# Kernel optimization log

Hardware: AMD Instinct MI355X
Metric: run time of the kernel (lower is better)

The kernel has to match this reference:

```python
import jax, jax.numpy as jnp
import numpy as np

B, M, EMBED, HEADS = 64, 1024, 1024, 8
HD = EMBED // HEADS  # 128
MID = 64             # att_mid_dim[1]
ALPHA = 1.3          # cfg.MODEL.BILINEAR.ELU_ALPHA (CELU)


def celu(x):
    return jax.nn.celu(x, alpha=ALPHA)


def group_norm(x, w, b, G=HEADS, eps=1e-5):
    # torch GroupNorm in source uses unbiased variance (ddof=1)
    N, C = x.shape
    xg = x.reshape(N, G, C // G)
    m = xg.mean(-1, keepdims=True)
    v = xg.var(-1, ddof=1, keepdims=True)
    xg = (xg - m) / jnp.sqrt(v + eps)
    return xg.reshape(N, C) * w + b


def setup_inputs() -> dict:
    key = jax.random.key(0)
    ks = jax.random.split(key, 16)
    s = 0.02
    return {
        "h_state": jax.random.normal(ks[0], (B, EMBED), jnp.float32),
        "att_feats": jax.random.normal(ks[1], (B, M, EMBED), jnp.float32),
        "att_mask": jnp.ones((B, M), jnp.float32),
        "p_att_feats": jax.random.normal(ks[2], (B, M, 2 * EMBED), jnp.float32),
        "Wq": jax.random.normal(ks[3], (EMBED, EMBED), jnp.float32) * s,
        "bq": jnp.zeros((EMBED,), jnp.float32),
        "gnw_q": jnp.ones((EMBED,), jnp.float32),
        "gnb_q": jnp.zeros((EMBED,), jnp.float32),
        "Wv1": jax.random.normal(ks[4], (EMBED, EMBED), jnp.float32) * s,
        "bv1": jnp.zeros((EMBED,), jnp.float32),
        "gnw_v1": jnp.ones((EMBED,), jnp.float32),
        "gnb_v1": jnp.zeros((EMBED,), jnp.float32),
        "Wb": jax.random.normal(ks[5], (HEADS, HD, MID), jnp.float32) * s,
        "bb": jax.random.normal(ks[6], (HEADS, MID), jnp.float32) * s,
        "Ws": jax.random.normal(ks[7], (HEADS, MID, 1), jnp.float32) * s,
        "bs": jax.random.normal(ks[8], (HEADS, 1), jnp.float32) * s,
        "Wc": jax.random.normal(ks[9], (HEADS, MID, HD), jnp.float32) * s,
        "bc": jax.random.normal(ks[10], (HEADS, HD), jnp.float32) * s,
        "Wt": jax.random.normal(ks[11], (2 * EMBED, EMBED), jnp.float32) * s,
        "bt": jnp.zeros((EMBED,), jnp.float32),
        "lnw": jnp.ones((EMBED,), jnp.float32),
        "lnb": jnp.zeros((EMBED,), jnp.float32),
    }


def reference(h_state, att_feats, att_mask, p_att_feats,
              Wq, bq, gnw_q, gnb_q, Wv1, bv1, gnw_v1, gnb_v1,
              Wb, bb, Ws, bs, Wc, bc, Wt, bt, lnw, lnb):
    b = h_state.shape[0]
    # precompute=True path: split p_att_feats into key / value2
    p_key = p_att_feats[..., :EMBED]
    p_value2 = p_att_feats[..., EMBED:]

    # q / v1 branches: Linear -> CELU -> GroupNorm
    q = group_norm(celu(h_state @ Wq + bq), gnw_q, gnb_q)    # [B, E]
    v1 = group_norm(celu(h_state @ Wv1 + bv1), gnw_v1, gnb_v1)

    p_query = q.reshape(b, HEADS, HD)[:, :, None, :]          # [B, H, 1, D]
    p_value1 = v1.reshape(b, HEADS, HD)[:, :, None, :]        # [B, H, 1, D]
    p_key = p_key.reshape(b, M, HEADS, HD).transpose(0, 2, 1, 3)     # [B, H, M, D]
    p_value2 = p_value2.reshape(b, M, HEADS, HD).transpose(0, 2, 1, 3)

    fusion = p_value2 * p_value1                              # [B, H, M, D]
    att_map = p_query * p_key                                 # [B, H, M, D]

    # attention_basic: MH_Linear + ReLU (dropout is identity at eval)
    am = jax.nn.relu(jnp.einsum('bhmi,hio->bhmo', att_map, Wb) + bb[None, :, None, :])  # [B,H,M,MID]

    mask = att_mask[:, None, :]                               # [B, 1, M]
    mext = mask[..., None]                                    # [B, 1, M, 1]
    att_map_pool = (am * mext).sum(-2) / mext.sum(-2)         # [B, H, MID]

    alpha_spatial = (jnp.einsum('bhmi,hio->bhmo', am, Ws) + bs[None, :, None, :])[..., 0]  # [B,H,M]
    alpha_spatial = jnp.where(mask == 0, -1e9, alpha_spatial)
    alpha_spatial = jax.nn.softmax(alpha_spatial, axis=-1)

    att = jnp.einsum('bhm,bhmd->bhd', alpha_spatial, fusion)  # [B, H, D]

    alpha_channel = jax.nn.sigmoid(jnp.einsum('bhi,hio->bho', att_map_pool, Wc) + bc[None])
    att = (att * alpha_channel).reshape(b, EMBED)

    out = jnp.concatenate([h_state, att], axis=-1) @ Wt + bt  # [B, E]
    mu = out.mean(-1, keepdims=True)
    var = out.var(-1, keepdims=True)
    out = (out - mu) / jnp.sqrt(var + 1e-5) * lnw + lnb
    return out
```

## Files before the change

kernel.cpp:

```cpp
#include <hip/hip_runtime.h>
#include <hip/hip_bf16.h>
#include <cmath>

#define NB 64
#define NM 1024
#define NE 1024
#define NH 8
#define NHD 128
#define NMID 64
#define CELU_ALPHA 1.3f

typedef __attribute__((ext_vector_type(8))) short bf16x8;
typedef __attribute__((ext_vector_type(4))) float f32x4;

__device__ __forceinline__ float celuf(float x) {
    return x > 0.f ? x : CELU_ALPHA * expm1f(x / CELU_ALPHA);
}

__device__ __forceinline__ short f2bf(float x) {
    __hip_bfloat16 b = __float2bfloat16(x);
    return *reinterpret_cast<short*>(&b);
}

__global__ __launch_bounds__(256) void a1_partial(
    const float* __restrict__ h, const float* __restrict__ Wq,
    const float* __restrict__ Wv1, float* __restrict__ partA)
{
    const int t = threadIdx.x;
    const int mat = blockIdx.x >> 8;
    const int kq = (blockIdx.x >> 5) & 7;
    const int cc = (blockIdx.x & 31) * 32;
    const int kbase = kq * 128;
    const float* __restrict__ W = mat ? Wv1 : Wq;

    __shared__ float hs[64][68];
    const int col = cc + (t & 31);
    const int rowg = t >> 5;

    float acc[8];
#pragma unroll
    for (int j = 0; j < 8; ++j) acc[j] = 0.f;

    for (int k0 = 0; k0 < 128; k0 += 64) {
        {
            const int r = t >> 2, b0 = (t & 3) * 16;
#pragma unroll
            for (int u = 0; u < 4; ++u) {
                float4 v = *(const float4*)&h[r * 1024 + kbase + k0 + b0 + 4 * u];
                *(float4*)&hs[r][b0 + 4 * u] = v;
            }
        }
        __syncthreads();
#pragma unroll 8
        for (int kl = 0; kl < 64; ++kl) {
            const float wv = W[(size_t)(kbase + k0 + kl) * 1024 + col];
#pragma unroll
            for (int j = 0; j < 8; ++j)
                acc[j] = fmaf(hs[rowg * 8 + j][kl], wv, acc[j]);
        }
        __syncthreads();
    }
    float* __restrict__ out = partA + (size_t)(mat * 8 + kq) * 65536;
#pragma unroll
    for (int j = 0; j < 8; ++j)
        out[(rowg * 8 + j) * 1024 + col] = acc[j];
}

__global__ __launch_bounds__(256) void a2_fused(
    const float* __restrict__ partA,
    const float* __restrict__ bq, const float* __restrict__ bv1,
    const float* __restrict__ gnw_q, const float* __restrict__ gnb_q,
    const float* __restrict__ gnw_v, const float* __restrict__ gnb_v,
    float* __restrict__ qbuf, float* __restrict__ v1buf)
{
    const int t = threadIdx.x;
    const int mat = blockIdx.x >> 6;
    const int row = blockIdx.x & 63;
    float* __restrict__ outb = mat ? v1buf : qbuf;
    const float* __restrict__ bias = mat ? bv1 : bq;
    const float* __restrict__ gw = mat ? gnw_v : gnw_q;
    const float* __restrict__ gb = mat ? gnb_v : gnb_q;

    float4 x = *(const float4*)&bias[t * 4];
#pragma unroll
    for (int kq = 0; kq < 8; ++kq) {
        const float4 p = *(const float4*)&partA[(size_t)(mat * 8 + kq) * 65536 + row * 1024 + t * 4];
        x.x += p.x; x.y += p.y; x.z += p.z; x.w += p.w;
    }
    x.x = celuf(x.x); x.y = celuf(x.y); x.z = celuf(x.z); x.w = celuf(x.w);

    float s = x.x + x.y + x.z + x.w;
#pragma unroll
    for (int m = 16; m >= 1; m >>= 1) s += __shfl_xor(s, m);
    const float mean = s * (1.f / 128.f);
    const float d0 = x.x - mean, d1 = x.y - mean, d2 = x.z - mean, d3 = x.w - mean;
    float ss = d0 * d0 + d1 * d1 + d2 * d2 + d3 * d3;
#pragma unroll
    for (int m = 16; m >= 1; m >>= 1) ss += __shfl_xor(ss, m);
    const float inv = rsqrtf(ss * (1.f / 127.f) + 1e-5f);
    const float4 w4 = *(const float4*)&gw[t * 4];
    const float4 b4 = *(const float4*)&gb[t * 4];
    float4 y;
    y.x = d0 * inv * w4.x + b4.x;
    y.y = d1 * inv * w4.y + b4.y;
    y.z = d2 * inv * w4.z + b4.z;
    y.w = d3 * inv * w4.w + b4.w;
    *(float4*)&outb[row * 1024 + t * 4] = y;
}

__global__ __launch_bounds__(256) void b0_wbq(
    const float* __restrict__ q, const float* __restrict__ Wb,
    short* __restrict__ wbq_g)
{
    const int bid = blockIdx.x;
    const int b = bid >> 3, h = bid & 7;
    const int t = threadIdx.x;
    __shared__ float q_lds[128];
    if (t < 128) q_lds[t] = q[b * 1024 + h * 128 + t];
    __syncthreads();

    const int o = t >> 2;
    const int i0 = (t & 3) * 32;
    union { short s[32]; uint4 q4[4]; } u;
#pragma unroll 8
    for (int v = 0; v < 32; ++v) {
        const int i = i0 + v;
        u.s[v] = f2bf(q_lds[i] * Wb[h * 8192 + i * 64 + o]);
    }
    uint4* dst = (uint4*)&wbq_g[(size_t)bid * 8192 + o * 128 + i0];
#pragma unroll
    for (int r = 0; r < 4; ++r) dst[r] = u.q4[r];
}

__global__ __launch_bounds__(256) void b_fused(
    const float* __restrict__ pat, const float* __restrict__ mask,
    const short* __restrict__ wbq_g,
    const float* __restrict__ bb, const float* __restrict__ Ws,
    const float* __restrict__ bs,
    float* __restrict__ pool_pt, float* __restrict__ esum_pt,
    float* __restrict__ av_pt)
{
    const int t = threadIdx.x;
    const int bid = blockIdx.x;
    const int b = bid >> 5;
    const int h = (bid >> 2) & 7;
    const int chunk = bid & 3;
    const int w = t >> 6;
    const int lane = t & 63;
    const int ln15 = lane & 15;
    const int lg = lane >> 4;
    const int dg = lane & 31;
    const int rwg = lane >> 5;

    __shared__ float mask_lds[256];
    __shared__ float e_lds[4][16];
    __shared__ float att_red[4][128];
    __shared__ float pool_red[4][64];
    __shared__ float esum_red[4];

    mask_lds[t] = mask[b * 1024 + chunk * 256 + t];

    const short* __restrict__ wb = wbq_g + (size_t)(bid >> 2) * 8192;
    bf16x8 bfr[4][4];
#pragma unroll
    for (int nt = 0; nt < 4; ++nt)
#pragma unroll
        for (int ks = 0; ks < 4; ++ks)
            bfr[nt][ks] = *(const bf16x8*)&wb[(nt * 16 + ln15) * 128 + ks * 32 + lg * 8];

    float wsr[4], bbr[4];
#pragma unroll
    for (int nt = 0; nt < 4; ++nt) {
        wsr[nt] = Ws[h * 64 + nt * 16 + ln15];
        bbr[nt] = bb[h * 64 + nt * 16 + ln15];
    }
    const float bsh = bs[h];
    float pool_part[4] = {0.f, 0.f, 0.f, 0.f};
    float esum_part = 0.f;
    float4 a4 = {0.f, 0.f, 0.f, 0.f};

    const float* __restrict__ patk = pat + (size_t)b * NM * 2048 + h * 128;
    const float* __restrict__ patv = patk + 1024;

    __syncthreads();

    for (int it = 0; it < 4; ++it) {
        const int ml0 = (w * 4 + it) * 16;
        const int m0 = chunk * 256 + ml0;

        const float* __restrict__ rowp = patk + (size_t)(m0 + ln15) * 2048 + lg * 8;
        bf16x8 af[4];
#pragma unroll
        for (int ks = 0; ks < 4; ++ks) {
            const float4 x = *(const float4*)(rowp + ks * 32);
            const float4 y = *(const float4*)(rowp + ks * 32 + 4);
            union { bf16x8 v; short s[8]; } u8;
            u8.s[0] = f2bf(x.x); u8.s[1] = f2bf(x.y);
            u8.s[2] = f2bf(x.z); u8.s[3] = f2bf(x.w);
            u8.s[4] = f2bf(y.x); u8.s[5] = f2bf(y.y);
            u8.s[6] = f2bf(y.z); u8.s[7] = f2bf(y.w);
            af[ks] = u8.v;
        }

        f32x4 acc[4];
#pragma unroll
        for (int nt = 0; nt < 4; ++nt) acc[nt] = (f32x4){0.f, 0.f, 0.f, 0.f};
#pragma unroll
        for (int ks = 0; ks < 4; ++ks)
#pragma unroll
            for (int nt = 0; nt < 4; ++nt)
                acc[nt] = __builtin_amdgcn_mfma_f32_16x16x32_bf16(af[ks], bfr[nt][ks], acc[nt], 0, 0, 0);

#pragma unroll
        for (int j = 0; j < 4; ++j) {
            const int ml = ml0 + lg * 4 + j;
            const float mk = mask_lds[ml];
            float sp = 0.f;
#pragma unroll
            for (int nt = 0; nt < 4; ++nt) {
                float a = acc[nt][j] + bbr[nt];
                a = fmaxf(a, 0.f);
                sp = fmaf(a, wsr[nt], sp);
                pool_part[nt] = fmaf(a, mk, pool_part[nt]);
            }
            sp += __shfl_xor(sp, 1);
            sp += __shfl_xor(sp, 2);
            sp += __shfl_xor(sp, 4);
            sp += __shfl_xor(sp, 8);
            if (ln15 == 0) {
                const float e = (mk == 0.f) ? 0.f : expf(sp + bsh);
                e_lds[w][lg * 4 + j] = e;
                esum_part += e;
            }
        }

        const float* __restrict__ vrow = patv + (size_t)(m0 + rwg) * 2048 + dg * 4;
#pragma unroll
        for (int r = 0; r < 8; ++r) {
            const float4 v = *(const float4*)(vrow + (size_t)(2 * r) * 2048);
            const float e = e_lds[w][rwg + 2 * r];
            a4.x = fmaf(e, v.x, a4.x);
            a4.y = fmaf(e, v.y, a4.y);
            a4.z = fmaf(e, v.z, a4.z);
            a4.w = fmaf(e, v.w, a4.w);
        }
    }

    a4.x += __shfl_xor(a4.x, 32);
    a4.y += __shfl_xor(a4.y, 32);
    a4.z += __shfl_xor(a4.z, 32);
    a4.w += __shfl_xor(a4.w, 32);
    if (lane < 32) *(float4*)&att_red[w][dg * 4] = a4;

#pragma unroll
    for (int nt = 0; nt < 4; ++nt) {
        float p = pool_part[nt];
        p += __shfl_xor(p, 16);
        p += __shfl_xor(p, 32);
        if (lane < 16) pool_red[w][nt * 16 + lane] = p;
    }

#pragma unroll
    for (int m = 32; m >= 1; m >>= 1) esum_part += __shfl_xor(esum_part, m);
    if (lane == 0) esum_red[w] = esum_part;
    __syncthreads();

    if (t < 128)
        av_pt[(size_t)bid * 128 + t] =
            att_red[0][t] + att_red[1][t] + att_red[2][t] + att_red[3][t];
    else if (t < 192)
        pool_pt[(size_t)bid * 64 + (t - 128)] =
            pool_red[0][t - 128] + pool_red[1][t - 128] + pool_red[2][t - 128] + pool_red[3][t - 128];
    else if (t == 192)
        esum_pt[bid] = esum_red[0] + esum_red[1] + esum_red[2] + esum_red[3];
}

__global__ __launch_bounds__(256) void b5_final(
    const float* __restrict__ pool_pt, const float* __restrict__ esum_pt,
    const float* __restrict__ av_pt, const float* __restrict__ mask,
    const float* __restrict__ Wc, const float* __restrict__ bc,
    const float* __restrict__ v1, float* __restrict__ att_out)
{
    const int t = threadIdx.x;
    const int bid = blockIdx.x;
    const int b = bid >> 3;
    const int h = bid & 7;
    const int w = t >> 6, lane = t & 63;

    __shared__ float red4[4];
    __shared__ float pool2[64];

    const float4 mk4 = *(const float4*)&mask[b * 1024 + t * 4];
    float msp = mk4.x + mk4.y + mk4.z + mk4.w;
#pragma unroll
    for (int m = 32; m >= 1; m >>= 1) msp += __shfl_xor(msp, m);
    if (lane == 0) red4[w] = msp;
    __syncthreads();
    const float msum = red4[0] + red4[1] + red4[2] + red4[3];

    if (t < 64) {
        const float pp = pool_pt[(size_t)(bid * 4) * 64 + t] + pool_pt[(size_t)(bid * 4 + 1) * 64 + t]
                       + pool_pt[(size_t)(bid * 4 + 2) * 64 + t] + pool_pt[(size_t)(bid * 4 + 3) * 64 + t];
        pool2[t] = pp / msum;
    }
    __syncthreads();

    if (t < 128) {
        const int d = t;
        const float av = av_pt[(size_t)(bid * 4) * 128 + d] + av_pt[(size_t)(bid * 4 + 1) * 128 + d]
                       + av_pt[(size_t)(bid * 4 + 2) * 128 + d] + av_pt[(size_t)(bid * 4 + 3) * 128 + d];
        const float esum = esum_pt[bid * 4] + esum_pt[bid * 4 + 1]
                         + esum_pt[bid * 4 + 2] + esum_pt[bid * 4 + 3];
        const float att = av / esum;
        float ac = bc[h * 128 + d];
#pragma unroll 8
        for (int o = 0; o < 64; ++o)
            ac = fmaf(pool2[o], Wc[h * 8192 + o * 128 + d], ac);
        const float sig = 1.f / (1.f + expf(-ac));
        att_out[b * 1024 + h * 128 + d] = att * sig * v1[b * 1024 + h * 128 + d];
    }
}

__global__ __launch_bounds__(256) void c1_partial(
    const float* __restrict__ h, const float* __restrict__ att,
    const float* __restrict__ Wt, float* __restrict__ part)
{
    const int t = threadIdx.x;
    const int kq = blockIdx.x >> 5;
    const int cc = (blockIdx.x & 31) * 32;
    const int col = cc + (t & 31);
    const int rowg = t >> 5;
    const float* __restrict__ x = (kq < 8) ? h : att;
    const int kbase = (kq & 7) * 128;

    __shared__ float xs[64][68];
    float acc[8];
#pragma unroll
    for (int j = 0; j < 8; ++j) acc[j] = 0.f;

    for (int k0 = 0; k0 < 128; k0 += 64) {
        {
            const int r = t >> 2, b0 = (t & 3) * 16;
#pragma unroll
            for (int u = 0; u < 4; ++u) {
                float4 v = *(const float4*)&x[r * 1024 + kbase + k0 + b0 + 4 * u];
                *(float4*)&xs[r][b0 + 4 * u] = v;
            }
        }
        __syncthreads();
#pragma unroll 8
        for (int kl = 0; kl < 64; ++kl) {
            const float wv = Wt[(size_t)(kq * 128 + k0 + kl) * 1024 + col];
#pragma unroll
            for (int j = 0; j < 8; ++j)
                acc[j] = fmaf(xs[rowg * 8 + j][kl], wv, acc[j]);
        }
        __syncthreads();
    }
#pragma unroll
    for (int j = 0; j < 8; ++j)
        part[(size_t)kq * 65536 + (rowg * 8 + j) * 1024 + col] = acc[j];
}

__global__ __launch_bounds__(256) void c2_ln(
    const float* __restrict__ part, const float* __restrict__ bt,
    const float* __restrict__ lnw, const float* __restrict__ lnb,
    float* __restrict__ out)
{
    const int t = threadIdx.x;
    const int row = blockIdx.x;
    const int w = t >> 6, lane = t & 63;
    __shared__ float red[4];

    float4 v = *(const float4*)&bt[t * 4];
#pragma unroll
    for (int qd = 0; qd < 16; ++qd) {
        const float4 p = *(const float4*)&part[(size_t)qd * 65536 + row * 1024 + t * 4];
        v.x += p.x; v.y += p.y; v.z += p.z; v.w += p.w;
    }
    float s = v.x + v.y + v.z + v.w;
#pragma unroll
    for (int m = 32; m >= 1; m >>= 1) s += __shfl_xor(s, m);
    if (lane == 0) red[w] = s;
    __syncthreads();
    const float mean = (red[0] + red[1] + red[2] + red[3]) * (1.f / 1024.f);
    __syncthreads();
    const float d0 = v.x - mean, d1 = v.y - mean, d2 = v.z - mean, d3 = v.w - mean;
    float ss = d0 * d0 + d1 * d1 + d2 * d2 + d3 * d3;
#pragma unroll
    for (int m = 32; m >= 1; m >>= 1) ss += __shfl_xor(ss, m);
    if (lane == 0) red[w] = ss;
    __syncthreads();
    const float var = (red[0] + red[1] + red[2] + red[3]) * (1.f / 1024.f);
    const float inv = rsqrtf(var + 1e-5f);
    const float4 w4 = *(const float4*)&lnw[t * 4];
    const float4 b4 = *(const float4*)&lnb[t * 4];
    float4 y;
    y.x = d0 * inv * w4.x + b4.x;
    y.y = d1 * inv * w4.y + b4.y;
    y.z = d2 * inv * w4.z + b4.z;
    y.w = d3 * inv * w4.w + b4.w;
    *(float4*)&out[row * 1024 + t * 4] = y;
}

extern "C" void kernel_launch(void* const* d_in, const int* in_sizes, int n_in,
                              void* d_out, int out_size, void* d_ws, size_t ws_size,
                              hipStream_t stream)
{
    const float* h_state  = (const float*)d_in[0];
    const float* att_mask = (const float*)d_in[2];
    const float* pat      = (const float*)d_in[3];
    const float* Wq       = (const float*)d_in[4];
    const float* bq       = (const float*)d_in[5];
    const float* gnw_q    = (const float*)d_in[6];
    const float* gnb_q    = (const float*)d_in[7];
    const float* Wv1      = (const float*)d_in[8];
    const float* bv1      = (const float*)d_in[9];
    const float* gnw_v1   = (const float*)d_in[10];
    const float* gnb_v1   = (const float*)d_in[11];
    const float* Wb       = (const float*)d_in[12];
    const float* bb       = (const float*)d_in[13];
    const float* Ws       = (const float*)d_in[14];
    const float* bs       = (const float*)d_in[15];
    const float* Wc       = (const float*)d_in[16];
    const float* bc       = (const float*)d_in[17];
    const float* Wt       = (const float*)d_in[18];
    const float* bt       = (const float*)d_in[19];
    const float* lnw      = (const float*)d_in[20];
    const float* lnb      = (const float*)d_in[21];
    float* out = (float*)d_out;

    float* ws      = (float*)d_ws;
    float* qbuf    = ws;
    float* v1buf   = ws + 65536;
    float* attb    = ws + 131072;
    float* parts   = ws + 196608;
    short* wbq_g   = (short*)(ws + 1245184);
    float* pool_pt = ws + 3342336;
    float* esum_pt = ws + 3473408;
    float* av_pt   = ws + 3475456;

    a1_partial<<<512, 256, 0, stream>>>(h_state, Wq, Wv1, parts);
    a2_fused<<<128, 256, 0, stream>>>(parts, bq, bv1, gnw_q, gnb_q, gnw_v1, gnb_v1,
                                      qbuf, v1buf);
    b0_wbq<<<512, 256, 0, stream>>>(qbuf, Wb, wbq_g);
    b_fused<<<2048, 256, 0, stream>>>(pat, att_mask, wbq_g, bb, Ws, bs,
                                      pool_pt, esum_pt, av_pt);
    b5_final<<<512, 256, 0, stream>>>(pool_pt, esum_pt, av_pt, att_mask,
                                      Wc, bc, v1buf, attb);
    c1_partial<<<512, 256, 0, stream>>>(h_state, attb, Wt, parts);
    c2_ln<<<64, 256, 0, stream>>>(parts, bt, lnw, lnb, out);
}
```

Baseline: 200.9 us.

## Retile small GEMMs, fuse group-norm into Wb prep, prefetch V rows

Result: faster. 160.8 us (-20.0%).

```diff
diff --git a/kernel.cpp b/kernel.cpp
--- a/kernel.cpp
+++ b/kernel.cpp
@@ -22,110 +22,118 @@
     return *reinterpret_cast<short*>(&b);
 }
 
-__global__ __launch_bounds__(256) void a1_partial(
+__global__ __launch_bounds__(256) void a1_tile(
     const float* __restrict__ h, const float* __restrict__ Wq,
     const float* __restrict__ Wv1, float* __restrict__ partA)
 {
     const int t = threadIdx.x;
-    const int mat = blockIdx.x >> 8;
-    const int kq = (blockIdx.x >> 5) & 7;
-    const int cc = (blockIdx.x & 31) * 32;
+    const int mat = blockIdx.x >> 7;
+    const int kq = (blockIdx.x >> 4) & 7;
+    const int cc = (blockIdx.x & 15) * 64;
     const int kbase = kq * 128;
     const float* __restrict__ W = mat ? Wv1 : Wq;
 
-    __shared__ float hs[64][68];
-    const int col = cc + (t & 31);
-    const int rowg = t >> 5;
-
-    float acc[8];
-#pragma unroll
-    for (int j = 0; j < 8; ++j) acc[j] = 0.f;
-
-    for (int k0 = 0; k0 < 128; k0 += 64) {
-        {
-            const int r = t >> 2, b0 = (t & 3) * 16;
-#pragma unroll
-            for (int u = 0; u < 4; ++u) {
-                float4 v = *(const float4*)&h[r * 1024 + kbase + k0 + b0 + 4 * u];
-                *(float4*)&hs[r][b0 + 4 * u] = v;
-            }
-        }
-        __syncthreads();
-#pragma unroll 8
-        for (int kl = 0; kl < 64; ++kl) {
-            const float wv = W[(size_t)(kbase + k0 + kl) * 1024 + col];
-#pragma unroll
-            for (int j = 0; j < 8; ++j)
-                acc[j] = fmaf(hs[rowg * 8 + j][kl], wv, acc[j]);
-        }
-        __syncthreads();
-    }
+    __shared__ float wl[128][64];
+    __shared__ float hl[64][132];
+
+#pragma unroll
+    for (int u = 0; u < 8; ++u) {
+        const int f = t + 256 * u;
+        const int row = f >> 4, c4 = f & 15;
+        *(float4*)&wl[row][c4 * 4] =
+            *(const float4*)&W[(size_t)(kbase + row) * 1024 + cc + c4 * 4];
+    }
+#pragma unroll
+    for (int u = 0; u < 8; ++u) {
+        const int f = t + 256 * u;
+        const int r = f >> 5, k4 = f & 31;
+        *(float4*)&hl[r][k4 * 4] = *(const float4*)&h[r * 1024 + kbase + k4 * 4];
+    }
+    __syncthreads();
+
+    const int r0 = (t >> 4) * 4;
+    const int c0 = (t & 15) * 4;
+    float acc[4][4];
+#pragma unroll
+    for (int i = 0; i < 4; ++i)
+#pragma unroll
+        for (int j = 0; j < 4; ++j) acc[i][j] = 0.f;
+
+#pragma unroll 4
+    for (int k = 0; k < 128; ++k) {
+        const float4 w4 = *(const float4*)&wl[k][c0];
+        const float h0 = hl[r0][k], h1 = hl[r0 + 1][k];
+        const float h2 = hl[r0 + 2][k], h3 = hl[r0 + 3][k];
+        acc[0][0] = fmaf(h0, w4.x, acc[0][0]); acc[0][1] = fmaf(h0, w4.y, acc[0][1]);
+        acc[0][2] = fmaf(h0, w4.z, acc[0][2]); acc[0][3] = fmaf(h0, w4.w, acc[0][3]);
+        acc[1][0] = fmaf(h1, w4.x, acc[1][0]); acc[1][1] = fmaf(h1, w4.y, acc[1][1]);
+        acc[1][2] = fmaf(h1, w4.z, acc[1][2]); acc[1][3] = fmaf(h1, w4.w, acc[1][3]);
+        acc[2][0] = fmaf(h2, w4.x, acc[2][0]); acc[2][1] = fmaf(h2, w4.y, acc[2][1]);
+        acc[2][2] = fmaf(h2, w4.z, acc[2][2]); acc[2][3] = fmaf(h2, w4.w, acc[2][3]);
+        acc[3][0] = fmaf(h3, w4.x, acc[3][0]); acc[3][1] = fmaf(h3, w4.y, acc[3][1]);
+        acc[3][2] = fmaf(h3, w4.z, acc[3][2]); acc[3][3] = fmaf(h3, w4.w, acc[3][3]);
+    }
+
     float* __restrict__ out = partA + (size_t)(mat * 8 + kq) * 65536;
 #pragma unroll
-    for (int j = 0; j < 8; ++j)
-        out[(rowg * 8 + j) * 1024 + col] = acc[j];
-}
-
-__global__ __launch_bounds__(256) void a2_fused(
+    for (int i = 0; i < 4; ++i) {
+        float4 v = {acc[i][0], acc[i][1], acc[i][2], acc[i][3]};
+        *(float4*)&out[(r0 + i) * 1024 + cc + c0] = v;
+    }
+}
+
+__global__ __launch_bounds__(256) void a2b0(
     const float* __restrict__ partA,
     const float* __restrict__ bq, const float* __restrict__ bv1,
     const float* __restrict__ gnw_q, const float* __restrict__ gnb_q,
     const float* __restrict__ gnw_v, const float* __restrict__ gnb_v,
-    float* __restrict__ qbuf, float* __restrict__ v1buf)
-{
-    const int t = threadIdx.x;
-    const int mat = blockIdx.x >> 6;
-    const int row = blockIdx.x & 63;
-    float* __restrict__ outb = mat ? v1buf : qbuf;
-    const float* __restrict__ bias = mat ? bv1 : bq;
-    const float* __restrict__ gw = mat ? gnw_v : gnw_q;
-    const float* __restrict__ gb = mat ? gnb_v : gnb_q;
-
-    float4 x = *(const float4*)&bias[t * 4];
-#pragma unroll
-    for (int kq = 0; kq < 8; ++kq) {
-        const float4 p = *(const float4*)&partA[(size_t)(mat * 8 + kq) * 65536 + row * 1024 + t * 4];
-        x.x += p.x; x.y += p.y; x.z += p.z; x.w += p.w;
-    }
-    x.x = celuf(x.x); x.y = celuf(x.y); x.z = celuf(x.z); x.w = celuf(x.w);
-
-    float s = x.x + x.y + x.z + x.w;
-#pragma unroll
-    for (int m = 16; m >= 1; m >>= 1) s += __shfl_xor(s, m);
-    const float mean = s * (1.f / 128.f);
-    const float d0 = x.x - mean, d1 = x.y - mean, d2 = x.z - mean, d3 = x.w - mean;
-    float ss = d0 * d0 + d1 * d1 + d2 * d2 + d3 * d3;
-#pragma unroll
-    for (int m = 16; m >= 1; m >>= 1) ss += __shfl_xor(ss, m);
-    const float inv = rsqrtf(ss * (1.f / 127.f) + 1e-5f);
-    const float4 w4 = *(const float4*)&gw[t * 4];
-    const float4 b4 = *(const float4*)&gb[t * 4];
-    float4 y;
-    y.x = d0 * inv * w4.x + b4.x;
-    y.y = d1 * inv * w4.y + b4.y;
-    y.z = d2 * inv * w4.z + b4.z;
-    y.w = d3 * inv * w4.w + b4.w;
-    *(float4*)&outb[row * 1024 + t * 4] = y;
-}
-
-__global__ __launch_bounds__(256) void b0_wbq(
-    const float* __restrict__ q, const float* __restrict__ Wb,
-    short* __restrict__ wbq_g)
+    const float* __restrict__ Wb,
+    float* __restrict__ v1buf, short* __restrict__ wbq_g)
 {
     const int bid = blockIdx.x;
-    const int b = bid >> 3, h = bid & 7;
-    const int t = threadIdx.x;
+    const int b = bid >> 3, hh = bid & 7;
+    const int t = threadIdx.x;
+    const int mat = t >> 7;
+    const int c = t & 127;
+    const int ch = hh * 128 + c;
+    const int w = t >> 6, lane = t & 63;
+
     __shared__ float q_lds[128];
-    if (t < 128) q_lds[t] = q[b * 1024 + h * 128 + t];
+    __shared__ float red[4][2];
+
+    float x = mat ? bv1[ch] : bq[ch];
+#pragma unroll
+    for (int kq = 0; kq < 8; ++kq)
+        x += partA[(size_t)(mat * 8 + kq) * 65536 + b * 1024 + ch];
+    x = celuf(x);
+
+    float s = x, s2 = x * x;
+#pragma unroll
+    for (int m = 32; m >= 1; m >>= 1) {
+        s += __shfl_xor(s, m);
+        s2 += __shfl_xor(s2, m);
+    }
+    if (lane == 0) { red[w][0] = s; red[w][1] = s2; }
+    __syncthreads();
+    const float S  = red[mat * 2][0] + red[mat * 2 + 1][0];
+    const float S2 = red[mat * 2][1] + red[mat * 2 + 1][1];
+    const float mean = S * (1.f / 128.f);
+    const float var = (S2 - 128.f * mean * mean) * (1.f / 127.f);
+    const float inv = rsqrtf(var + 1e-5f);
+    const float gw = mat ? gnw_v[ch] : gnw_q[ch];
+    const float gb = mat ? gnb_v[ch] : gnb_q[ch];
+    const float y = (x - mean) * inv * gw + gb;
+    if (mat == 0) q_lds[c] = y;
+    else v1buf[b * 1024 + ch] = y;
     __syncthreads();
 
     const int o = t >> 2;
     const int i0 = (t & 3) * 32;
-    union { short s[32]; uint4 q4[4]; } u;
+    union { short sv[32]; uint4 q4[4]; } u;
 #pragma unroll 8
     for (int v = 0; v < 32; ++v) {
         const int i = i0 + v;
-        u.s[v] = f2bf(q_lds[i] * Wb[h * 8192 + i * 64 + o]);
+        u.sv[v] = f2bf(q_lds[i] * Wb[hh * 8192 + i * 64 + o]);
     }
     uint4* dst = (uint4*)&wbq_g[(size_t)bid * 8192 + o * 128 + i0];
 #pragma unroll
@@ -189,16 +197,26 @@
         const int m0 = chunk * 256 + ml0;
 
         const float* __restrict__ rowp = patk + (size_t)(m0 + ln15) * 2048 + lg * 8;
+        float4 ax[4], ay[4];
+#pragma unroll
+        for (int ks = 0; ks < 4; ++ks) {
+            ax[ks] = *(const float4*)(rowp + ks * 32);
+            ay[ks] = *(const float4*)(rowp + ks * 32 + 4);
+        }
+        const float* __restrict__ vrow = patv + (size_t)(m0 + rwg) * 2048 + dg * 4;
+        float4 vv[8];
+#pragma unroll
+        for (int r = 0; r < 8; ++r)
+            vv[r] = *(const float4*)(vrow + (size_t)(2 * r) * 2048);
+
         bf16x8 af[4];
 #pragma unroll
         for (int ks = 0; ks < 4; ++ks) {
-            const float4 x = *(const float4*)(rowp + ks * 32);
-            const float4 y = *(const float4*)(rowp + ks * 32 + 4);
             union { bf16x8 v; short s[8]; } u8;
-            u8.s[0] = f2bf(x.x); u8.s[1] = f2bf(x.y);
-            u8.s[2] = f2bf(x.z); u8.s[3] = f2bf(x.w);
-            u8.s[4] = f2bf(y.x); u8.s[5] = f2bf(y.y);
-            u8.s[6] = f2bf(y.z); u8.s[7] = f2bf(y.w);
+            u8.s[0] = f2bf(ax[ks].x); u8.s[1] = f2bf(ax[ks].y);
+            u8.s[2] = f2bf(ax[ks].z); u8.s[3] = f2bf(ax[ks].w);
+            u8.s[4] = f2bf(ay[ks].x); u8.s[5] = f2bf(ay[ks].y);
+            u8.s[6] = f2bf(ay[ks].z); u8.s[7] = f2bf(ay[ks].w);
             af[ks] = u8.v;
         }
 
@@ -234,15 +252,13 @@
             }
         }
 
-        const float* __restrict__ vrow = patv + (size_t)(m0 + rwg) * 2048 + dg * 4;
 #pragma unroll
         for (int r = 0; r < 8; ++r) {
-            const float4 v = *(const float4*)(vrow + (size_t)(2 * r) * 2048);
             const float e = e_lds[w][rwg + 2 * r];
-            a4.x = fmaf(e, v.x, a4.x);
-            a4.y = fmaf(e, v.y, a4.y);
-            a4.z = fmaf(e, v.z, a4.z);
-            a4.w = fmaf(e, v.w, a4.w);
+            a4.x = fmaf(e, vv[r].x, a4.x);
+            a4.y = fmaf(e, vv[r].y, a4.y);
+            a4.z = fmaf(e, vv[r].z, a4.z);
+            a4.w = fmaf(e, vv[r].w, a4.w);
         }
     }
 
@@ -321,45 +337,62 @@
     }
 }
 
-__global__ __launch_bounds__(256) void c1_partial(
+__global__ __launch_bounds__(256) void c1_tile(
     const float* __restrict__ h, const float* __restrict__ att,
     const float* __restrict__ Wt, float* __restrict__ part)
 {
     const int t = threadIdx.x;
-    const int kq = blockIdx.x >> 5;
-    const int cc = (blockIdx.x & 31) * 32;
-    const int col = cc + (t & 31);
-    const int rowg = t >> 5;
+    const int kq = blockIdx.x >> 4;
+    const int cc = (blockIdx.x & 15) * 64;
     const float* __restrict__ x = (kq < 8) ? h : att;
     const int kbase = (kq & 7) * 128;
 
-    __shared__ float xs[64][68];
-    float acc[8];
-#pragma unroll
-    for (int j = 0; j < 8; ++j) acc[j] = 0.f;
-
-    for (int k0 = 0; k0 < 128; k0 += 64) {
-        {
-            const int r = t >> 2, b0 = (t & 3) * 16;
-#pragma unroll
-            for (int u = 0; u < 4; ++u) {
-                float4 v = *(const float4*)&x[r * 1024 + kbase + k0 + b0 + 4 * u];
-                *(float4*)&xs[r][b0 + 4 * u] = v;
-            }
-        }
-        __syncthreads();
-#pragma unroll 8
-        for (int kl = 0; kl < 64; ++kl) {
-            const float wv = Wt[(size_t)(kq * 128 + k0 + kl) * 1024 + col];
-#pragma unroll
-            for (int j = 0; j < 8; ++j)
-                acc[j] = fmaf(xs[rowg * 8 + j][kl], wv, acc[j]);
-        }
-        __syncthreads();
-    }
-#pragma unroll
-    for (int j = 0; j < 8; ++j)
-        part[(size_t)kq * 65536 + (rowg * 8 + j) * 1024 + col] = acc[j];
+    __shared__ float wl[128][64];
+    __shared__ float hl[64][132];
+
+#pragma unroll
+    for (int u = 0; u < 8; ++u) {
+        const int f = t + 256 * u;
+        const int row = f >> 4, c4 = f & 15;
+        *(float4*)&wl[row][c4 * 4] =
+            *(const float4*)&Wt[(size_t)(kq * 128 + row) * 1024 + cc + c4 * 4];
+    }
+#pragma unroll
+    for (int u = 0; u < 8; ++u) {
+        const int f = t + 256 * u;
+        const int r = f >> 5, k4 = f & 31;
+        *(float4*)&hl[r][k4 * 4] = *(const float4*)&x[r * 1024 + kbase + k4 * 4];
+    }
+    __syncthreads();
+
+    const int r0 = (t >> 4) * 4;
+    const int c0 = (t & 15) * 4;
+    float acc[4][4];
+#pragma unroll
+    for (int i = 0; i < 4; ++i)
+#pragma unroll
+        for (int j = 0; j < 4; ++j) acc[i][j] = 0.f;
+
+#pragma unroll 4
+    for (int k = 0; k < 128; ++k) {
+        const float4 w4 = *(const float4*)&wl[k][c0];
+        const float h0 = hl[r0][k], h1 = hl[r0 + 1][k];
+        const float h2 = hl[r0 + 2][k], h3 = hl[r0 + 3][k];
+        acc[0][0] = fmaf(h0, w4.x, acc[0][0]); acc[0][1] = fmaf(h0, w4.y, acc[0][1]);
+        acc[0][2] = fmaf(h0, w4.z, acc[0][2]); acc[0][3] = fmaf(h0, w4.w, acc[0][3]);
+        acc[1][0] = fmaf(h1, w4.x, acc[1][0]); acc[1][1] = fmaf(h1, w4.y, acc[1][1]);
+        acc[1][2] = fmaf(h1, w4.z, acc[1][2]); acc[1][3] = fmaf(h1, w4.w, acc[1][3]);
+        acc[2][0] = fmaf(h2, w4.x, acc[2][0]); acc[2][1] = fmaf(h2, w4.y, acc[2][1]);
+        acc[2][2] = fmaf(h2, w4.z, acc[2][2]); acc[2][3] = fmaf(h2, w4.w, acc[2][3]);
+        acc[3][0] = fmaf(h3, w4.x, acc[3][0]); acc[3][1] = fmaf(h3, w4.y, acc[3][1]);
+        acc[3][2] = fmaf(h3, w4.z, acc[3][2]); acc[3][3] = fmaf(h3, w4.w, acc[3][3]);
+    }
+
+#pragma unroll
+    for (int i = 0; i < 4; ++i) {
+        float4 v = {acc[i][0], acc[i][1], acc[i][2], acc[i][3]};
+        *(float4*)&part[(size_t)kq * 65536 + (r0 + i) * 1024 + cc + c0] = v;
+    }
 }
 
 __global__ __launch_bounds__(256) void c2_ln(
@@ -431,23 +464,21 @@
     float* out = (float*)d_out;
 
     float* ws      = (float*)d_ws;
-    float* qbuf    = ws;
-    float* v1buf   = ws + 65536;
-    float* attb    = ws + 131072;
-    float* parts   = ws + 196608;
-    short* wbq_g   = (short*)(ws + 1245184);
-    float* pool_pt = ws + 3342336;
-    float* esum_pt = ws + 3473408;
-    float* av_pt   = ws + 3475456;
-
-    a1_partial<<<512, 256, 0, stream>>>(h_state, Wq, Wv1, parts);
-    a2_fused<<<128, 256, 0, stream>>>(parts, bq, bv1, gnw_q, gnb_q, gnw_v1, gnb_v1,
-                                      qbuf, v1buf);
-    b0_wbq<<<512, 256, 0, stream>>>(qbuf, Wb, wbq_g);
+    float* v1buf   = ws;
+    float* attb    = ws + 65536;
+    float* parts   = ws + 131072;
+    short* wbq_g   = (short*)(ws + 1179648);
+    float* pool_pt = ws + 3276800;
+    float* esum_pt = ws + 3407872;
+    float* av_pt   = ws + 3409920;
+
+    a1_tile<<<256, 256, 0, stream>>>(h_state, Wq, Wv1, parts);
+    a2b0<<<512, 256, 0, stream>>>(parts, bq, bv1, gnw_q, gnb_q, gnw_v1, gnb_v1,
+                                  Wb, v1buf, wbq_g);
     b_fused<<<2048, 256, 0, stream>>>(pat, att_mask, wbq_g, bb, Ws, bs,
                                       pool_pt, esum_pt, av_pt);
     b5_final<<<512, 256, 0, stream>>>(pool_pt, esum_pt, av_pt, att_mask,
                                       Wc, bc, v1buf, attb);
-    c1_partial<<<512, 256, 0, stream>>>(h_state, attb, Wt, parts);
+    c1_tile<<<256, 256, 0, stream>>>(h_state, attb, Wt, parts);
     c2_ln<<<64, 256, 0, stream>>>(parts, bt, lnw, lnb, out);
 }
```
